# Optimization experiments

Hardware: AMD Instinct MI355X
Metric: run time of the kernel (lower is better)

The kernel has to match this reference:

```python
import jax, jax.numpy as jnp
import numpy as np

HEADS = 16
DIM_HEAD = 64
SCALE = DIM_HEAD ** -0.5
EPS = 1e-5


def _bitlinear(x, w):
    """BitNet b1.58 BitLinear (kyegomez/BitNet), eval-mode, bias-free.
    w: [out, in] torch-layout. Ternary weight quant (scale = mean|w|),
    per-token int8 absmax activation quant, straight-through estimator.
    """
    ws = 1.0 / jnp.clip(jnp.mean(jnp.abs(w)), EPS, None)
    wq = jnp.clip(jnp.round(w * ws), -1.0, 1.0) / ws
    wq = w + jax.lax.stop_gradient(wq - w)
    xs = 127.0 / jnp.clip(jnp.max(jnp.abs(x), axis=-1, keepdims=True), EPS, None)
    xq = jnp.clip(jnp.round(x * xs), -128.0, 127.0) / xs
    xq = x + jax.lax.stop_gradient(xq - x)
    return jnp.einsum('bnd,od->bno', xq, wq)


def setup_inputs() -> dict:
    key = jax.random.key(0)
    ks = jax.random.split(key, 6)
    b, n, d = 2, 2048, 1024
    return {
        'x': jax.random.normal(ks[0], (b, n, d), dtype=jnp.float32),
        'context': jax.random.normal(ks[1], (b, n, d), dtype=jnp.float32),
        'Wq': jax.random.normal(ks[2], (d, d), dtype=jnp.float32) * 0.02,
        'Wk': jax.random.normal(ks[3], (d, d), dtype=jnp.float32) * 0.02,
        'Wv': jax.random.normal(ks[4], (d, d), dtype=jnp.float32) * 0.02,
        'Wo': jax.random.normal(ks[5], (d, d), dtype=jnp.float32) * 0.02,
    }


def reference(x, context, Wq, Wk, Wv, Wo):
    b, n, _ = x.shape
    m = context.shape[1]
    q = _bitlinear(x, Wq)
    k = _bitlinear(context, Wk)
    v = _bitlinear(context, Wv)
    # b n (h d) -> b h n d
    q = q.reshape(b, n, HEADS, DIM_HEAD).transpose(0, 2, 1, 3)
    k = k.reshape(b, m, HEADS, DIM_HEAD).transpose(0, 2, 1, 3)
    v = v.reshape(b, m, HEADS, DIM_HEAD).transpose(0, 2, 1, 3)
    dots = jnp.einsum('bhid,bhjd->bhij', q, k) * SCALE
    attn = jax.nn.softmax(dots, axis=-1)  # dropout is identity in eval
    out = jnp.einsum('bhij,bhjd->bhid', attn, v)
    out = out.transpose(0, 2, 1, 3).reshape(b, n, HEADS * DIM_HEAD)
    return _bitlinear(out, Wo)
```

## Files before the change

kernel.cpp:

```cpp
#include <hip/hip_runtime.h>
#include <math.h>

#define HEADS   16
#define DHEAD   64
#define SEQ     2048
#define NB      2
#define DM      1024
#define NTOK    4096
#define WEPS    1e-5

using f16x8   = __attribute__((ext_vector_type(8))) _Float16;
using f16x4   = __attribute__((ext_vector_type(4))) _Float16;
using floatx4 = __attribute__((ext_vector_type(4))) float;
using i32x4   = __attribute__((ext_vector_type(4))) int;

typedef __attribute__((address_space(1))) unsigned int gu32;
typedef __attribute__((address_space(3))) unsigned int lu32;

#define BAR_LGKM()  asm volatile("s_waitcnt lgkmcnt(0)\n\ts_barrier" ::: "memory")
#define WAIT_LGKM() asm volatile("s_waitcnt lgkmcnt(0)" ::: "memory")

__device__ __forceinline__ unsigned short h16b(_Float16 h) {
    union { _Float16 h; unsigned short u; } c; c.h = h; return c.u;
}

__global__ void wsum1(const float* __restrict__ w0, const float* __restrict__ w1,
                      const float* __restrict__ w2, const float* __restrict__ w3,
                      double* __restrict__ partial) {
    const float* w = (blockIdx.y == 0) ? w0 : (blockIdx.y == 1) ? w1 : (blockIdx.y == 2) ? w2 : w3;
    int base = blockIdx.x * 16384;
    double s = 0.0;
    for (int i = threadIdx.x; i < 16384; i += 256)
        s += fabs((double)w[base + i]);
    __shared__ double sd[256];
    sd[threadIdx.x] = s;
    __syncthreads();
    for (int st = 128; st > 0; st >>= 1) {
        if (threadIdx.x < st) sd[threadIdx.x] += sd[threadIdx.x + st];
        __syncthreads();
    }
    if (threadIdx.x == 0) partial[blockIdx.y * 64 + blockIdx.x] = sd[0];
}

__global__ void wsum2(const double* __restrict__ partial, double* __restrict__ wscale) {
    int t = threadIdx.x;
    if (t < 4) {
        double s = 0.0;
        for (int i = 0; i < 64; i++) s += partial[t * 64 + i];
        double mean = s / (1024.0 * 1024.0);
        wscale[t] = (mean > WEPS) ? mean : WEPS;
    }
}

__global__ void wquant(const float* __restrict__ w0, const float* __restrict__ w1,
                       const float* __restrict__ w2, const float* __restrict__ w3,
                       const double* __restrict__ wscale, signed char* __restrict__ wq) {
    int widx = blockIdx.y;
    const float* w = (widx == 0) ? w0 : (widx == 1) ? w1 : (widx == 2) ? w2 : w3;
    double ws = 1.0 / wscale[widx];
    int idx = (blockIdx.x * 256 + threadIdx.x) * 4;
    float4 wv = *(const float4*)(w + idx);
    char4 o;
    {
        double r = rint((double)wv.x * ws); r = r > 1.0 ? 1.0 : (r < -1.0 ? -1.0 : r); o.x = (signed char)r;
    } {
        double r = rint((double)wv.y * ws); r = r > 1.0 ? 1.0 : (r < -1.0 ? -1.0 : r); o.y = (signed char)r;
    } {
        double r = rint((double)wv.z * ws); r = r > 1.0 ? 1.0 : (r < -1.0 ? -1.0 : r); o.z = (signed char)r;
    } {
        double r = rint((double)wv.w * ws); r = r > 1.0 ? 1.0 : (r < -1.0 ? -1.0 : r); o.w = (signed char)r;
    }
    *(char4*)(wq + (size_t)widx * 1048576 + idx) = o;
}

__device__ __forceinline__ void aquant_row(const float* __restrict__ row,
                                           signed char* __restrict__ dst_row,
                                           double* __restrict__ ascale_p) {
    int t = threadIdx.x;
    float4 xv = *(const float4*)(row + t * 4);
    float a = fmaxf(fmaxf(fabsf(xv.x), fabsf(xv.y)), fmaxf(fabsf(xv.z), fabsf(xv.w)));
    __shared__ float sm[256];
    sm[t] = a;
    __syncthreads();
    for (int st = 128; st > 0; st >>= 1) {
        if (t < st) sm[t] = fmaxf(sm[t], sm[t + st]);
        __syncthreads();
    }
    double mx = (double)sm[0];
    if (mx < WEPS) mx = WEPS;
    if (t == 0) *ascale_p = mx / 127.0;
    double xs = 127.0 / mx;
    char4 o;
    {
        double r = rint((double)xv.x * xs); r = r > 127.0 ? 127.0 : (r < -128.0 ? -128.0 : r); o.x = (signed char)r;
    } {
        double r = rint((double)xv.y * xs); r = r > 127.0 ? 127.0 : (r < -128.0 ? -128.0 : r); o.y = (signed char)r;
    } {
        double r = rint((double)xv.z * xs); r = r > 127.0 ? 127.0 : (r < -128.0 ? -128.0 : r); o.z = (signed char)r;
    } {
        double r = rint((double)xv.w * xs); r = r > 127.0 ? 127.0 : (r < -128.0 ? -128.0 : r); o.w = (signed char)r;
    }
    *(char4*)(dst_row + t * 4) = o;
}

__global__ void aquant(const float* __restrict__ src, signed char* __restrict__ dst,
                       double* __restrict__ ascale) {
    int tok = blockIdx.x;
    aquant_row(src + (size_t)tok * DM, dst + (size_t)tok * DM, ascale + tok);
}

__global__ void aquant2(const float* __restrict__ x, const float* __restrict__ ctx,
                        signed char* __restrict__ dst, double* __restrict__ ascale) {
    int tok = blockIdx.x;
    const float* row = (tok < NTOK) ? x + (size_t)tok * DM : ctx + (size_t)(tok - NTOK) * DM;
    aquant_row(row, dst + (size_t)tok * DM, ascale + tok);
}

__device__ __forceinline__ void gemm_core(
        const signed char* __restrict__ A, const signed char* __restrict__ W,
        const double* __restrict__ ascale, double wsc,
        void* __restrict__ outp, int mode, float prescale, int bx, int by) {
    __shared__ __align__(16) signed char lds_a[128 * 64];
    __shared__ __align__(16) signed char lds_b[128 * 64];
    const int tid  = threadIdx.x;
    const int wave = tid >> 6, lane = tid & 63;
    const int wr = wave >> 1, wc = wave & 1;
    const int quad = lane >> 4, l15 = lane & 15;
    const int row0 = by * 128, col0 = bx * 128;
    i32x4 acc[4][4] = {};

    const signed char* ga0 = A + (size_t)(row0 + (lane >> 2)) * DM + (lane & 3) * 16;
    const signed char* gb0 = W + (size_t)(col0 + (lane >> 2)) * DM + (lane & 3) * 16;

    for (int k0 = 0; k0 < DM; k0 += 64) {
        __syncthreads();
        #pragma unroll
        for (int t = 0; t < 2; t++) {
            const int i = wave + t * 4;
            __builtin_amdgcn_global_load_lds(
                (const gu32*)(const void*)(ga0 + (size_t)i * 16 * DM + k0),
                (lu32*)(void*)(lds_a + i * 1024), 16, 0, 0);
            __builtin_amdgcn_global_load_lds(
                (const gu32*)(const void*)(gb0 + (size_t)i * 16 * DM + k0),
                (lu32*)(void*)(lds_b + i * 1024), 16, 0, 0);
        }
        __syncthreads();
        i32x4 af[4], bfr[4];
        #pragma unroll
        for (int mi = 0; mi < 4; mi++) {
            int r = wr * 64 + mi * 16 + l15;
            af[mi] = *(const i32x4*)&lds_a[r * 64 + quad * 16];
        }
        #pragma unroll
        for (int ni = 0; ni < 4; ni++) {
            int n = wc * 64 + ni * 16 + l15;
            bfr[ni] = *(const i32x4*)&lds_b[n * 64 + quad * 16];
        }
        #pragma unroll
        for (int mi = 0; mi < 4; mi++)
            #pragma unroll
            for (int ni = 0; ni < 4; ni++)
                acc[mi][ni] = __builtin_amdgcn_mfma_i32_16x16x64_i8(af[mi], bfr[ni], acc[mi][ni], 0, 0, 0);
    }

    #pragma unroll
    for (int mi = 0; mi < 4; mi++) {
        int tbase = row0 + wr * 64 + mi * 16 + quad * 4;
        #pragma unroll
        for (int reg = 0; reg < 4; reg++) {
            int t = tbase + reg;
            double sa = ascale[t] * wsc;
            #pragma unroll
            for (int ni = 0; ni < 4; ni++) {
                int o = col0 + wc * 64 + ni * 16 + l15;
                float val = (float)((double)acc[mi][ni][reg] * sa);
                if (mode == 1) {
                    ((float*)outp)[(size_t)t * DM + o] = val;
                } else {
                    int bb = t >> 11, n = t & 2047, hh = o >> 6, dh = o & 63;
                    float fv = val * prescale;
                    _Float16 hl = (_Float16)fv;
                    _Float16 ml = (_Float16)((fv - (float)hl) * 2048.0f);
                    if (mode == 0) {
                        size_t idx = (((size_t)(bb * HEADS + hh) * SEQ + n) << 6) + dh;
                        ((unsigned short*)outp)[idx]           = h16b(hl);
                        ((unsigned short*)outp)[idx + 4194304] = h16b(ml);
                    } else {
                        size_t idx = (((size_t)(bb * HEADS + hh) * 64 + dh) << 11) + n;
                        ((unsigned short*)outp)[idx]           = h16b(hl);
                        ((unsigned short*)outp)[idx + 4194304] = h16b(ml);
                    }
                }
            }
        }
    }
}

__global__ __launch_bounds__(256) void gemm_qkv(
        const signed char* __restrict__ xq, const signed char* __restrict__ cq,
        const signed char* __restrict__ wqb, const double* __restrict__ ascale_x,
        const double* __restrict__ wscale, void* __restrict__ qkv) {
    const int which = blockIdx.x >> 3;
    char* base = (char*)qkv + (size_t)which * 16777216;
    gemm_core(which == 0 ? xq : cq,
              wqb + (size_t)which * 1048576,
              ascale_x + (which ? NTOK : 0),
              wscale[which],
              base,
              which == 2 ? 2 : 0,
              which == 0 ? 0.18033688011112042f : 1.0f, blockIdx.x & 7, blockIdx.y);
}

__global__ __launch_bounds__(256) void gemm_o(
        const signed char* __restrict__ aq, const signed char* __restrict__ wo,
        const double* __restrict__ ascale, const double* __restrict__ wscale_p,
        float* __restrict__ out) {
    gemm_core(aq, wo, ascale, *wscale_p, out, 1, 1.0f, blockIdx.x, blockIdx.y);
}

#define KH_IDX(row, d8) (((row) * 8 + ((d8) ^ ((row) & 7))) * 8)
#define VSW(row) (((row) >> 1) & 3)

__global__ __launch_bounds__(256, 4) void attn_mfma(
        const unsigned short* __restrict__ qhg, const unsigned short* __restrict__ qlg,
        const unsigned short* __restrict__ khg, const unsigned short* __restrict__ klg,
        const unsigned short* __restrict__ vhg, const unsigned short* __restrict__ vlg,
        float* __restrict__ out) {
    __shared__ __align__(16) _Float16 KhL[32 * 64];
    __shared__ __align__(16) _Float16 KlL[32 * 64];
    __shared__ __align__(16) _Float16 VhL[64 * 32];
    __shared__ __align__(16) _Float16 VlL[64 * 32];
    __shared__ __align__(16) _Float16 PhL[4][16 * 36];
    __shared__ __align__(16) _Float16 PlL[4][16 * 36];
    __shared__ float Lp[4][16][4];

    const int lin  = blockIdx.x;
    const int bh   = (lin & 7) * 4 + (lin >> 8);
    const int qblk = (lin >> 3) & 31;
    const int tid  = threadIdx.x;
    const int wave = tid >> 6, lane = tid & 63;
    const int l15  = lane & 15, quad = lane >> 4;
    const int qbase = qblk * 64 + wave * 16;

    f16x8 qh[2], qm[2];
    #pragma unroll
    for (int c = 0; c < 2; c++) {
        size_t off = (((size_t)bh * SEQ + qbase + l15) << 6) + c * 32 + quad * 8;
        qh[c] = *(const f16x8*)(qhg + off);
        qm[c] = *(const f16x8*)(qlg + off);
    }

    floatx4 och[4] = {};
    floatx4 ocm[4] = {};
    float lsum = 0.f;

    const unsigned short* khb = khg + ((size_t)bh * SEQ << 6);
    const unsigned short* klb = klg + ((size_t)bh * SEQ << 6);
    const unsigned short* vhb = vhg + ((size_t)bh << 17);
    const unsigned short* vlb = vlg + ((size_t)bh << 17);

    const int kk = tid >> 3, d8 = tid & 7;
    const int vrow = tid >> 2, vc = tid & 3;
    const int vcs  = vc ^ VSW(vrow);
    const unsigned short* vsh = vhb + ((size_t)vrow << 11) + vc * 8;
    const unsigned short* vsl = vlb + ((size_t)vrow << 11) + vc * 8;

    uint4 kh_pf = *(const uint4*)(khb + ((size_t)kk << 6) + d8 * 8);
    uint4 kl_pf = *(const uint4*)(klb + ((size_t)kk << 6) + d8 * 8);
    uint4 vh_pf = *(const uint4*)(vsh);
    uint4 vl_pf = *(const uint4*)(vsl);

    for (int kt = 0; kt < SEQ; kt += 32) {
        BAR_LGKM();

        *(uint4*)&KhL[KH_IDX(kk, d8)] = kh_pf;
        *(uint4*)&KlL[KH_IDX(kk, d8)] = kl_pf;
        *(uint4*)&VhL[(vrow * 4 + vcs) * 8] = vh_pf;
        *(uint4*)&VlL[(vrow * 4 + vcs) * 8] = vl_pf;

        if (kt + 32 < SEQ) {
            kh_pf = *(const uint4*)(khb + ((size_t)(kt + 32 + kk) << 6) + d8 * 8);
            kl_pf = *(const uint4*)(klb + ((size_t)(kt + 32 + kk) << 6) + d8 * 8);
            vh_pf = *(const uint4*)(vsh + kt + 32);
            vl_pf = *(const uint4*)(vsl + kt + 32);
        }

        BAR_LGKM();

        f16x8 kfh[2][2], kfl[2][2];
        #pragma unroll
        for (int ms = 0; ms < 2; ms++) {
            #pragma unroll
            for (int c = 0; c < 2; c++) {
                kfh[ms][c] = *(const f16x8*)&KhL[KH_IDX(ms * 16 + l15, c * 4 + quad)];
                kfl[ms][c] = *(const f16x8*)&KlL[KH_IDX(ms * 16 + l15, c * 4 + quad)];
            }
        }

        #pragma unroll
        for (int ms = 0; ms < 2; ms++) {
            floatx4 ah = {}, am = {};
            #pragma unroll
            for (int c = 0; c < 2; c++) {
                ah = __builtin_amdgcn_mfma_f32_16x16x32_f16(kfh[ms][c], qh[c], ah, 0, 0, 0);
                am = __builtin_amdgcn_mfma_f32_16x16x32_f16(kfh[ms][c], qm[c], am, 0, 0, 0);
                am = __builtin_amdgcn_mfma_f32_16x16x32_f16(kfl[ms][c], qh[c], am, 0, 0, 0);
            }
            float p[4];
            #pragma unroll
            for (int r = 0; r < 4; r++) {
                float s = ah[r] + am[r] * 4.8828125e-4f;
                p[r] = exp2f(s);
                lsum += p[r];
            }
            f16x4 hv, lv;
            #pragma unroll
            for (int r = 0; r < 4; r++) {
                _Float16 h = (_Float16)p[r];
                hv[r] = h;
                lv[r] = (_Float16)((p[r] - (float)h) * 2048.0f);
            }
            int poff = l15 * 36 + ms * 16 + quad * 4;
            *(f16x4*)&PhL[wave][poff] = hv;
            *(f16x4*)&PlL[wave][poff] = lv;
        }
        WAIT_LGKM();

        f16x8 pfh = *(const f16x8*)&PhL[wave][l15 * 36 + quad * 8];
        f16x8 pfm = *(const f16x8*)&PlL[wave][l15 * 36 + quad * 8];
        #pragma unroll
        for (int nh = 0; nh < 4; nh++) {
            int vro = nh * 16 + l15;
            int vof = (vro * 4 + (quad ^ VSW(vro))) * 8;
            f16x8 vfh = *(const f16x8*)&VhL[vof];
            f16x8 vfm = *(const f16x8*)&VlL[vof];
            och[nh] = __builtin_amdgcn_mfma_f32_16x16x32_f16(pfh, vfh, och[nh], 0, 0, 0);
            ocm[nh] = __builtin_amdgcn_mfma_f32_16x16x32_f16(pfh, vfm, ocm[nh], 0, 0, 0);
            ocm[nh] = __builtin_amdgcn_mfma_f32_16x16x32_f16(pfm, vfh, ocm[nh], 0, 0, 0);
        }
    }

    Lp[wave][l15][quad] = lsum;
    WAIT_LGKM();

    int b = bh >> 4, h = bh & 15;
    float linv[4];
    #pragma unroll
    for (int r = 0; r < 4; r++) {
        float4 lv = *(const float4*)&Lp[wave][quad * 4 + r][0];
        linv[r] = 1.0f / (lv.x + lv.y + lv.z + lv.w);
    }
    #pragma unroll
    for (int nh = 0; nh < 4; nh++) {
        #pragma unroll
        for (int r = 0; r < 4; r++) {
            int token = b * SEQ + qbase + quad * 4 + r;
            float val = (och[nh][r] + ocm[nh][r] * 4.8828125e-4f) * linv[r];
            out[(size_t)token * DM + h * 64 + nh * 16 + l15] = val;
        }
    }
}

extern "C" void kernel_launch(void* const* d_in, const int* in_sizes, int n_in,
                              void* d_out, int out_size, void* d_ws, size_t ws_size,
                              hipStream_t stream) {
    const float* x       = (const float*)d_in[0];
    const float* context = (const float*)d_in[1];
    const float* Wq      = (const float*)d_in[2];
    const float* Wk      = (const float*)d_in[3];
    const float* Wv      = (const float*)d_in[4];
    const float* Wo      = (const float*)d_in[5];
    char* ws = (char*)d_ws;

    double* wscale   = (double*)(ws + 0);
    double* partial  = (double*)(ws + 4096);
    double* ascale_x = (double*)(ws + 8192);
    double* ascale_a = (double*)(ws + 73728);
    signed char* wqb = (signed char*)(ws + 131072);
    signed char* xq  = (signed char*)(ws + 4325376);
    signed char* cq  = (signed char*)(ws + 8519680);
    float* attn_out  = (float*)(ws + 4325376);
    char* planes     = ws + 21102592;
    signed char* aq  = (signed char*)(ws + 21102592);

    unsigned short* qhg = (unsigned short*)planes;
    unsigned short* qlg = qhg + 4194304;
    unsigned short* khg = (unsigned short*)(planes + 16777216);
    unsigned short* klg = khg + 4194304;
    unsigned short* vhg = (unsigned short*)(planes + 33554432);
    unsigned short* vlg = vhg + 4194304;

    wsum1<<<dim3(64, 4), 256, 0, stream>>>(Wq, Wk, Wv, Wo, partial);
    wsum2<<<1, 64, 0, stream>>>(partial, wscale);
    wquant<<<dim3(1024, 4), 256, 0, stream>>>(Wq, Wk, Wv, Wo, wscale, wqb);
    aquant2<<<2 * NTOK, 256, 0, stream>>>(x, context, xq, ascale_x);

    gemm_qkv<<<dim3(24, 32), 256, 0, stream>>>(xq, cq, wqb, ascale_x, wscale, planes);

    attn_mfma<<<dim3(1024), 256, 0, stream>>>(qhg, qlg, khg, klg, vhg, vlg, attn_out);

    aquant<<<NTOK, 256, 0, stream>>>(attn_out, aq, ascale_a);
    gemm_o<<<dim3(8, 32), 256, 0, stream>>>(aq, wqb + 3145728, ascale_a, wscale + 3, (float*)d_out);
}
```

Measured before the change: 317.8 us.

## Load V fragments directly from global memory and vectorize transposed V stores

```diff
diff --git a/kernel.cpp b/kernel.cpp
--- a/kernel.cpp
+++ b/kernel.cpp
@@ -166,27 +166,44 @@
     #pragma unroll
     for (int mi = 0; mi < 4; mi++) {
         int tbase = row0 + wr * 64 + mi * 16 + quad * 4;
-        #pragma unroll
-        for (int reg = 0; reg < 4; reg++) {
-            int t = tbase + reg;
-            double sa = ascale[t] * wsc;
+        if (mode == 2) {
+            int bb = tbase >> 11, n = tbase & 2047;
             #pragma unroll
             for (int ni = 0; ni < 4; ni++) {
                 int o = col0 + wc * 64 + ni * 16 + l15;
-                float val = (float)((double)acc[mi][ni][reg] * sa);
-                if (mode == 1) {
-                    ((float*)outp)[(size_t)t * DM + o] = val;
-                } else {
-                    int bb = t >> 11, n = t & 2047, hh = o >> 6, dh = o & 63;
-                    float fv = val * prescale;
+                int hh = o >> 6, dh = o & 63;
+                ushort4 hv, lv;
+                #pragma unroll
+                for (int reg = 0; reg < 4; reg++) {
+                    int t = tbase + reg;
+                    double sa = ascale[t] * wsc;
+                    float fv = (float)((double)acc[mi][ni][reg] * sa) * prescale;
                     _Float16 hl = (_Float16)fv;
                     _Float16 ml = (_Float16)((fv - (float)hl) * 2048.0f);
-                    if (mode == 0) {
+                    ((unsigned short*)&hv)[reg] = h16b(hl);
+                    ((unsigned short*)&lv)[reg] = h16b(ml);
+                }
+                size_t idx = (((size_t)(bb * HEADS + hh) * 64 + dh) << 11) + n;
+                *(ushort4*)((unsigned short*)outp + idx)           = hv;
+                *(ushort4*)((unsigned short*)outp + idx + 4194304) = lv;
+            }
+        } else {
+            #pragma unroll
+            for (int reg = 0; reg < 4; reg++) {
+                int t = tbase + reg;
+                double sa = ascale[t] * wsc;
+                #pragma unroll
+                for (int ni = 0; ni < 4; ni++) {
+                    int o = col0 + wc * 64 + ni * 16 + l15;
+                    float val = (float)((double)acc[mi][ni][reg] * sa);
+                    if (mode == 1) {
+                        ((float*)outp)[(size_t)t * DM + o] = val;
+                    } else {
+                        int bb = t >> 11, n = t & 2047, hh = o >> 6, dh = o & 63;
+                        float fv = val * prescale;
+                        _Float16 hl = (_Float16)fv;
+                        _Float16 ml = (_Float16)((fv - (float)hl) * 2048.0f);
                         size_t idx = (((size_t)(bb * HEADS + hh) * SEQ + n) << 6) + dh;
-                        ((unsigned short*)outp)[idx]           = h16b(hl);
-                        ((unsigned short*)outp)[idx + 4194304] = h16b(ml);
-                    } else {
-                        size_t idx = (((size_t)(bb * HEADS + hh) * 64 + dh) << 11) + n;
                         ((unsigned short*)outp)[idx]           = h16b(hl);
                         ((unsigned short*)outp)[idx + 4194304] = h16b(ml);
                     }
@@ -219,7 +236,6 @@
 }
 
 #define KH_IDX(row, d8) (((row) * 8 + ((d8) ^ ((row) & 7))) * 8)
-#define VSW(row) (((row) >> 1) & 3)
 
 __global__ __launch_bounds__(256, 4) void attn_mfma(
         const unsigned short* __restrict__ qhg, const unsigned short* __restrict__ qlg,
@@ -228,15 +244,13 @@
         float* __restrict__ out) {
     __shared__ __align__(16) _Float16 KhL[32 * 64];
     __shared__ __align__(16) _Float16 KlL[32 * 64];
-    __shared__ __align__(16) _Float16 VhL[64 * 32];
-    __shared__ __align__(16) _Float16 VlL[64 * 32];
     __shared__ __align__(16) _Float16 PhL[4][16 * 36];
     __shared__ __align__(16) _Float16 PlL[4][16 * 36];
     __shared__ float Lp[4][16][4];
 
     const int lin  = blockIdx.x;
-    const int bh   = (lin & 7) * 4 + (lin >> 8);
-    const int qblk = (lin >> 3) & 31;
+    const int bh   = (lin & 7) * 4 + ((lin >> 3) & 3);
+    const int qblk = (lin >> 5) & 31;
     const int tid  = threadIdx.x;
     const int wave = tid >> 6, lane = tid & 63;
     const int l15  = lane & 15, quad = lane >> 4;
@@ -260,29 +274,19 @@
     const unsigned short* vlb = vlg + ((size_t)bh << 17);
 
     const int kk = tid >> 3, d8 = tid & 7;
-    const int vrow = tid >> 2, vc = tid & 3;
-    const int vcs  = vc ^ VSW(vrow);
-    const unsigned short* vsh = vhb + ((size_t)vrow << 11) + vc * 8;
-    const unsigned short* vsl = vlb + ((size_t)vrow << 11) + vc * 8;
 
     uint4 kh_pf = *(const uint4*)(khb + ((size_t)kk << 6) + d8 * 8);
     uint4 kl_pf = *(const uint4*)(klb + ((size_t)kk << 6) + d8 * 8);
-    uint4 vh_pf = *(const uint4*)(vsh);
-    uint4 vl_pf = *(const uint4*)(vsl);
 
     for (int kt = 0; kt < SEQ; kt += 32) {
         BAR_LGKM();
 
         *(uint4*)&KhL[KH_IDX(kk, d8)] = kh_pf;
         *(uint4*)&KlL[KH_IDX(kk, d8)] = kl_pf;
-        *(uint4*)&VhL[(vrow * 4 + vcs) * 8] = vh_pf;
-        *(uint4*)&VlL[(vrow * 4 + vcs) * 8] = vl_pf;
 
         if (kt + 32 < SEQ) {
             kh_pf = *(const uint4*)(khb + ((size_t)(kt + 32 + kk) << 6) + d8 * 8);
             kl_pf = *(const uint4*)(klb + ((size_t)(kt + 32 + kk) << 6) + d8 * 8);
-            vh_pf = *(const uint4*)(vsh + kt + 32);
-            vl_pf = *(const uint4*)(vsl + kt + 32);
         }
 
         BAR_LGKM();
@@ -297,19 +301,33 @@
             }
         }
 
+        floatx4 ah[2], am[2];
         #pragma unroll
         for (int ms = 0; ms < 2; ms++) {
-            floatx4 ah = {}, am = {};
+            ah[ms] = (floatx4){};
+            am[ms] = (floatx4){};
             #pragma unroll
             for (int c = 0; c < 2; c++) {
-                ah = __builtin_amdgcn_mfma_f32_16x16x32_f16(kfh[ms][c], qh[c], ah, 0, 0, 0);
-                am = __builtin_amdgcn_mfma_f32_16x16x32_f16(kfh[ms][c], qm[c], am, 0, 0, 0);
-                am = __builtin_amdgcn_mfma_f32_16x16x32_f16(kfl[ms][c], qh[c], am, 0, 0, 0);
-            }
+                ah[ms] = __builtin_amdgcn_mfma_f32_16x16x32_f16(kfh[ms][c], qh[c], ah[ms], 0, 0, 0);
+                am[ms] = __builtin_amdgcn_mfma_f32_16x16x32_f16(kfh[ms][c], qm[c], am[ms], 0, 0, 0);
+                am[ms] = __builtin_amdgcn_mfma_f32_16x16x32_f16(kfl[ms][c], qh[c], am[ms], 0, 0, 0);
+            }
+        }
+
+        f16x8 vfh[4], vfm[4];
+        #pragma unroll
+        for (int nh = 0; nh < 4; nh++) {
+            size_t voff = (((size_t)(nh * 16 + l15)) << 11) + kt + quad * 8;
+            vfh[nh] = *(const f16x8*)(vhb + voff);
+            vfm[nh] = *(const f16x8*)(vlb + voff);
+        }
+
+        #pragma unroll
+        for (int ms = 0; ms < 2; ms++) {
             float p[4];
             #pragma unroll
             for (int r = 0; r < 4; r++) {
-                float s = ah[r] + am[r] * 4.8828125e-4f;
+                float s = ah[ms][r] + am[ms][r] * 4.8828125e-4f;
                 p[r] = exp2f(s);
                 lsum += p[r];
             }
@@ -330,13 +348,9 @@
         f16x8 pfm = *(const f16x8*)&PlL[wave][l15 * 36 + quad * 8];
         #pragma unroll
         for (int nh = 0; nh < 4; nh++) {
-            int vro = nh * 16 + l15;
-            int vof = (vro * 4 + (quad ^ VSW(vro))) * 8;
-            f16x8 vfh = *(const f16x8*)&VhL[vof];
-            f16x8 vfm = *(const f16x8*)&VlL[vof];
-            och[nh] = __builtin_amdgcn_mfma_f32_16x16x32_f16(pfh, vfh, och[nh], 0, 0, 0);
-            ocm[nh] = __builtin_amdgcn_mfma_f32_16x16x32_f16(pfh, vfm, ocm[nh], 0, 0, 0);
-            ocm[nh] = __builtin_amdgcn_mfma_f32_16x16x32_f16(pfm, vfh, ocm[nh], 0, 0, 0);
+            och[nh] = __builtin_amdgcn_mfma_f32_16x16x32_f16(pfh, vfh[nh], och[nh], 0, 0, 0);
+            ocm[nh] = __builtin_amdgcn_mfma_f32_16x16x32_f16(pfh, vfm[nh], ocm[nh], 0, 0, 0);
+            ocm[nh] = __builtin_amdgcn_mfma_f32_16x16x32_f16(pfm, vfh[nh], ocm[nh], 0, 0, 0);
         }
     }
 
```

Measured after the change: 418.2 us. 31.6% more time.
